# Kernel optimization log

Measured on AMD Instinct MI355X. Metric: run time of the kernel, lower is better.

The kernel has to match this reference:

```python
import jax, jax.numpy as jnp
from jax import lax
import numpy as np

K = 5  # length_inter_tile
EPS = 0.01


def _conv(x, w, b):
    y = lax.conv_general_dilated(x, w, (1, 1), ((1, 1), (1, 1)),
                                 dimension_numbers=('NCHW', 'OIHW', 'NCHW'))
    return y + b[None, :, None, None]


def _leaky(x):
    return jnp.where(x >= 0, x, 0.01 * x)


def _unfold(x, k=K):
    # torch F.unfold(x, k, padding=k//2): (b,c,h,w) -> (b, c*k*k, h*w), channel-major ordering
    b, c, h, w = x.shape
    p = k // 2
    xp = jnp.pad(x, ((0, 0), (0, 0), (p, p), (p, p)))
    pat = jnp.stack([xp[:, :, i:i + h, j:j + w] for i in range(k) for j in range(k)], axis=2)
    return pat.reshape(b, c * k * k, h * w)


def _fold(x, c, h, w, k=K):
    # torch F.fold: (b, c*k*k, h*w) -> (b, c, h, w) with overlap-add, padding=k//2
    b = x.shape[0]
    p = k // 2
    xr = x.reshape(b, c, k, k, h, w)
    out = jnp.zeros((b, c, h + 2 * p, w + 2 * p), x.dtype)
    for i in range(k):
        for j in range(k):
            out = out.at[:, :, i:i + h, j:j + w].add(xr[:, :, i, j])
    return out[:, :, p:p + h, p:p + w]


def _mmn(x, axes):
    mn = jnp.min(x, axis=axes, keepdims=True)
    mx = jnp.max(x, axis=axes, keepdims=True)
    return (x - mn) / (mx - mn + 0.001)


def setup_inputs() -> dict:
    key = jax.random.key(0)
    ks = jax.random.split(key, 8)
    b, t, ch_in, h, w = 1, 16, 10, 24, 24
    t_de, ch_de = 16, 12
    sc = 0.02
    return {
        'x': jax.random.normal(ks[0], (b, t, ch_in, h, w), jnp.float32),
        'design': jax.random.uniform(ks[1], (b, t_de, ch_de, h, w), jnp.float32),
        'gt': jax.random.uniform(ks[2], (b, t_de, 3, h, w), jnp.float32),
        'w1': jax.random.normal(ks[3], (1024, 160, 3, 3), jnp.float32) * sc,
        'b1': jnp.zeros((1024,), jnp.float32),
        'w2': jax.random.normal(ks[4], (1024, 1024, 3, 3), jnp.float32) * sc,
        'b2': jnp.zeros((1024,), jnp.float32),
        'w3': jax.random.normal(ks[5], (1024, 1024, 3, 3), jnp.float32) * sc,
        'b3': jnp.zeros((1024,), jnp.float32),
        'wf': jax.random.normal(ks[6], (6400, 1024, 3, 3), jnp.float32) * sc,
        'bf': jnp.zeros((6400,), jnp.float32),
    }


def _forward(x, design, gt, w1, b1, w2, b2, w3, b3, wf, bf):
    b, t, ch_in, h, w = x.shape
    t_de, ch_de = design.shape[1], design.shape[2]
    hw = h * w
    N = K * K  # num_inter

    # unfold design: (b, t_de*ch_de*N, hw) -> (b*hw, N, t_de, ch_de)
    d = _unfold(design.reshape(b, t_de * ch_de, h, w))
    d = d.transpose(0, 2, 1).reshape(b * hw, t_de * ch_de, N)
    d = d.transpose(0, 2, 1).reshape(b * hw, N, t_de, ch_de)

    # norm in each prediction window (per channel-group, per sample)
    d = jnp.concatenate([
        d[..., 0:1],
        _mmn(d[..., 1:4], (1, 2, 3)),
        _mmn(d[..., 4:5], (1, 2)),
        _mmn(d[..., 5:8], (1, 2, 3)),
        _mmn(d[..., 8:], (1, 2)),  # each grid channel independently
    ], axis=-1)

    M = b * hw * N
    domain = d.reshape(M, t_de, ch_de)
    X = d[:, :, :t, :].reshape(M, t, ch_de)

    # feature network (n_layers=4 -> 3 leaky convs) + weight head
    f = _leaky(_conv(x.reshape(b, t * ch_in, h, w), w1, b1))
    f = _leaky(_conv(f, w2, b2))
    f = _leaky(_conv(f, w3, b3))
    Wt = jnp.tanh(_conv(f, wf, bf))  # (b, N*t*t, h, w)
    Wm = Wt.reshape(b, N, t, t, h, w).transpose(0, 4, 5, 1, 2, 3).reshape(M, t, t)
    Wm = jnp.einsum('nij,nkj->nik', Wm, Wm) + jnp.eye(t, dtype=Wm.dtype)

    XTW = jnp.einsum('ntc,ntu->ncu', X, Wm)          # (M, ch_de, t)
    XTWX = jnp.einsum('nct,ntd->ncd', XTW, X)        # (M, ch_de, ch_de)
    A = XTWX.reshape(b * hw, N, ch_de, ch_de).sum(1) + EPS * jnp.eye(ch_de, dtype=XTWX.dtype)

    # reference for loss (unfolded)
    ref = _unfold(gt.reshape(b, t_de * 3, h, w))
    ref = ref.transpose(0, 2, 1).reshape(b * hw, t_de * 3, N)
    ref = ref.transpose(0, 2, 1).reshape(M, t_de, 3)

    outs, folded = [], []
    for ch in range(3):
        Y = _unfold(x[:, :, ch])                      # (b, t*N, hw)
        Y = Y.transpose(0, 2, 1).reshape(b * hw, t, N)
        Y = Y.transpose(0, 2, 1).reshape(M, t, 1)
        XTWY = jnp.einsum('nct,nto->nco', XTW, Y)
        Bv = XTWY.reshape(b * hw, N, ch_de, 1).sum(1)
        para = jnp.linalg.solve(A, Bv)                # (b*hw, ch_de, 1)
        para_r = jnp.broadcast_to(para[:, None], (b * hw, N, ch_de, 1)).reshape(M, ch_de, 1)
        o = jnp.einsum('ntc,nco->nto', domain, para_r)  # (M, t_de, 1)
        outs.append(o[..., 0])
        # overlap-add fold of per-window predictions
        oc = o.reshape(b, hw, N, t_de).transpose(0, 3, 2, 1).reshape(b, t_de * N, hw)
        num = _fold(oc, t_de, h, w)
        den = _fold(jnp.ones_like(oc), t_de, h, w)
        folded.append(num / den)

    out_for_loss = jnp.stack(outs, axis=-1)           # (M, t_de, 3)
    out = jnp.stack(folded, axis=2)                   # (b, t_de, 3, h, w)
    loss = jnp.mean(jnp.abs(out_for_loss - ref))      # L1 stand-in for loss_for_stit_v1
    return out, loss


def reference(x, design, gt, w1, b1, w2, b2, w3, b3, wf, bf):
    return _forward(x, design, gt, w1, b1, w2, b2, w3, b3, wf, bf)
```

## Files before the change

### kernel.cpp

```cpp
#include <hip/hip_runtime.h>
#include <math.h>


typedef __attribute__((ext_vector_type(8))) short sh8;
typedef __attribute__((ext_vector_type(4))) float f32x4;


__device__ inline void glds16(const void* gsrc, void* ldst) {
    __builtin_amdgcn_global_load_lds((const __attribute__((address_space(1))) void*)gsrc,
                                     (__attribute__((address_space(3))) void*)ldst, 16, 0, 0);
}

__global__ __launch_bounds__(64) void minmax_kernel(const float* __restrict__ design,
                                                    float* __restrict__ mn_o,
                                                    float* __restrict__ mx_o) {
    int p = blockIdx.x;
    int py = p / 24, px = p % 24;
    int lane = threadIdx.x;
    float mn[7], mx[7];
#pragma unroll
    for (int g = 0; g < 7; g++) { mn[g] = 1e30f; mx[g] = -1e30f; }
    for (int e = lane; e < 400; e += 64) {
        int n = e / 16, td = e % 16;
        int yy = py + n / 5 - 2, xx = px + n % 5 - 2;
        bool ok = (yy >= 0 && yy < 24 && xx >= 0 && xx < 24);
#pragma unroll
        for (int cd = 1; cd < 12; cd++) {
            float v = ok ? design[(td * 12 + cd) * 576 + yy * 24 + xx] : 0.0f;
            int g = (cd <= 3) ? 0 : (cd == 4) ? 1 : (cd <= 7) ? 2 : 3 + (cd - 8);
            mn[g] = fminf(mn[g], v);
            mx[g] = fmaxf(mx[g], v);
        }
    }
#pragma unroll
    for (int s = 32; s >= 1; s >>= 1) {
#pragma unroll
        for (int g = 0; g < 7; g++) {
            mn[g] = fminf(mn[g], __shfl_xor(mn[g], s));
            mx[g] = fmaxf(mx[g], __shfl_xor(mx[g], s));
        }
    }
    if (lane == 0) {
#pragma unroll
        for (int g = 0; g < 7; g++) {
            mn_o[p * 7 + g] = mn[g];
            mx_o[p * 7 + g] = mx[g];
        }
    }
}

__global__ void dnorm_kernel(const float* __restrict__ design,
                             const float* __restrict__ mn,
                             const float* __restrict__ mx,
                             float* __restrict__ dn) {
    int idx = blockIdx.x * 256 + threadIdx.x;
    if (idx >= 14400 * 192) return;
    int cd = idx % 12;
    int td = (idx / 12) % 16;
    int n  = (idx / 192) % 25;
    int p  = idx / 4800;
    int py = p / 24, px = p % 24;
    int yy = py + n / 5 - 2, xx = px + n % 5 - 2;
    float v = (yy >= 0 && yy < 24 && xx >= 0 && xx < 24)
                  ? design[(td * 12 + cd) * 576 + yy * 24 + xx] : 0.0f;
    if (cd >= 1) {
        int g = (cd <= 3) ? 0 : (cd == 4) ? 1 : (cd <= 7) ? 2 : 3 + (cd - 8);
        float a = mn[p * 7 + g], b = mx[p * 7 + g];
        v = (v - a) / (b - a + 0.001f);
    }
    dn[idx] = v;
}

__global__ __launch_bounds__(256) void im2col_kernel(const float* __restrict__ act,
                                                     char* __restrict__ x2t, int nrows) {
    int row = blockIdx.x * 256 + threadIdx.x;
    if (row >= nrows) return;
    int kc = row / 576, px = row % 576;
    int y = px / 24, x = px % 24;
    int k0 = kc * 32;
    int ic = k0 / 9;
    int tap = k0 - ic * 9;
    sh8 hv[4], lv[4];
#pragma unroll
    for (int e = 0; e < 32; ++e) {
        int dy = tap / 3, dx = tap - dy * 3;
        int yy = y + dy - 1, xx = x + dx - 1;
        float v = (yy >= 0 && yy < 24 && xx >= 0 && xx < 24)
                      ? act[ic * 576 + yy * 24 + xx] : 0.0f;
        unsigned u = __builtin_bit_cast(unsigned, v);
        hv[e / 8][e % 8] = (short)(u >> 16);
        float fh = __builtin_bit_cast(float, u & 0xFFFF0000u);
        lv[e / 8][e % 8] = (short)(__builtin_bit_cast(unsigned, v - fh) >> 16);
        if (++tap == 9) { tap = 0; ++ic; }
    }
    char* dst = x2t + (long)kc * 92160 + (long)px * 80;
#pragma unroll
    for (int s4 = 0; s4 < 4; ++s4) {
        *(sh8*)(dst + s4 * 16) = hv[s4];
        *(sh8*)(dst + 46080 + s4 * 16) = lv[s4];
    }
}

__global__ void finalize_kernel(const float* __restrict__ part,
                                const float* __restrict__ bias,
                                float* __restrict__ act, int total, int nsplit) {
    int idx = blockIdx.x * 256 + threadIdx.x;
    if (idx >= total) return;
    float s = 0.0f;
    for (int k = 0; k < nsplit; k++) s += part[(long)k * total + idx];
    s += bias[idx / 576];
    act[idx] = s >= 0.0f ? s : 0.01f * s;
}

template<int SWZ>
__global__ __launch_bounds__(256, 2)
void conv_mfma5_kernel(const char* __restrict__ x2t,
                       const float* __restrict__ wgt,
                       float* __restrict__ part,
                       int K, int cps, int cout) {
    __shared__ __align__(1024) char sB[46080];
    __shared__ __align__(1024) char sA[2][16384];

    const int tid = threadIdx.x;
    const int lane = tid & 63;
    const int w = tid >> 6;
    const int wo = w >> 1, wp = w & 1;
    const int q = lane >> 4, ln15 = lane & 15;

    int ocb, pxh, s;
    if (SWZ) {
        int g = blockIdx.x;
        int xcd = g & 7, slot = g >> 3;
        int p = xcd + 8 * (slot >> 1);
        ocb = p % 50; s = p / 50; pxh = slot & 1;
    } else {
        ocb = blockIdx.x; pxh = blockIdx.y; s = blockIdx.z;
    }
    const int c0 = s * cps;

    const int st_oc = tid >> 1;
    const int st_h  = tid & 1;
    const float* wrow = wgt + (long)(ocb * 128 + st_oc) * K + st_h * 16;
    const int wslot0 = (((st_h * 2 + 0) + (st_oc >> 1)) & 3) << 4;
    const int wslot1 = (((st_h * 2 + 1) + (st_oc >> 1)) & 3) << 4;
    char* const arow_base = (char*)nullptr;

    int aoff[4];
#pragma unroll
    for (int ot = 0; ot < 4; ++ot) {
        int oc = wo * 64 + ot * 16 + ln15;
        aoff[ot] = oc * 64 + (((q + (oc >> 1)) & 3) << 4);
    }
    const int bbase = (wp * 144 + ln15) * 80 + q * 16;

    f32x4 acc[4][9];
#pragma unroll
    for (int a = 0; a < 4; ++a)
#pragma unroll
        for (int j = 0; j < 9; ++j) acc[a][j] = f32x4{0.f, 0.f, 0.f, 0.f};

    {
        const float* p = wrow + (long)c0 * 32;
        float4 a0 = *(const float4*)(p);
        float4 a1 = *(const float4*)(p + 4);
        float4 a2 = *(const float4*)(p + 8);
        float4 a3 = *(const float4*)(p + 12);
        float av[16] = {a0.x, a0.y, a0.z, a0.w, a1.x, a1.y, a1.z, a1.w,
                        a2.x, a2.y, a2.z, a2.w, a3.x, a3.y, a3.z, a3.w};
        sh8 h8[2], l8[2];
#pragma unroll
        for (int e = 0; e < 16; ++e) {
            unsigned u = __builtin_bit_cast(unsigned, av[e]);
            h8[e / 8][e % 8] = (short)(u >> 16);
            float fh = __builtin_bit_cast(float, u & 0xFFFF0000u);
            l8[e / 8][e % 8] = (short)(__builtin_bit_cast(unsigned, av[e] - fh) >> 16);
        }
        char* hb = sA[0] + st_oc * 64;
        *(sh8*)(hb + wslot0) = h8[0];
        *(sh8*)(hb + wslot1) = h8[1];
        *(sh8*)(hb + 8192 + wslot0) = l8[0];
        *(sh8*)(hb + 8192 + wslot1) = l8[1];
    }

#pragma unroll 1
    for (int t = 0; t < cps; ++t) {
        const int cc = c0 + t;
        __syncthreads();
        {
            const char* bsrc = x2t + (long)cc * 92160 + pxh * 23040;
            for (int it = w; it < 45; it += 4) {
                int boff = it * 1024 + lane * 16;
                const char* src = (boff < 23040) ? bsrc + boff
                                                 : bsrc + 46080 + (boff - 23040);
                glds16(src, sB + it * 1024);
            }
        }
        __builtin_amdgcn_sched_barrier(0);
        const bool pf = (t + 1 < cps);
        float4 a0, a1, a2, a3;
        if (pf) {
            const float* p = wrow + (long)(cc + 1) * 32;
            a0 = *(const float4*)(p);
            a1 = *(const float4*)(p + 4);
            a2 = *(const float4*)(p + 8);
            a3 = *(const float4*)(p + 12);
            asm volatile("s_waitcnt vmcnt(4)" ::: "memory");
        } else {
            asm volatile("s_waitcnt vmcnt(0)" ::: "memory");
        }
        __syncthreads();

        const char* sAc = sA[t & 1];
        sh8 ah[4], al[4];
#pragma unroll
        for (int ot = 0; ot < 4; ++ot) {
            ah[ot] = *(const sh8*)(sAc + aoff[ot]);
            al[ot] = *(const sh8*)(sAc + 8192 + aoff[ot]);
        }
#pragma unroll
        for (int j = 0; j < 9; ++j) {
            int ba = bbase + j * (16 * 80);
            sh8 bh = *(const sh8*)(sB + ba);
            sh8 bl = *(const sh8*)(sB + 23040 + ba);
#pragma unroll
            for (int ot = 0; ot < 4; ++ot) {
                acc[ot][j] = __builtin_amdgcn_mfma_f32_16x16x32_bf16(ah[ot], bh, acc[ot][j], 0, 0, 0);
                acc[ot][j] = __builtin_amdgcn_mfma_f32_16x16x32_bf16(al[ot], bh, acc[ot][j], 0, 0, 0);
                acc[ot][j] = __builtin_amdgcn_mfma_f32_16x16x32_bf16(ah[ot], bl, acc[ot][j], 0, 0, 0);
            }
        }
        if (pf) {
            float av[16] = {a0.x, a0.y, a0.z, a0.w, a1.x, a1.y, a1.z, a1.w,
                            a2.x, a2.y, a2.z, a2.w, a3.x, a3.y, a3.z, a3.w};
            sh8 h8[2], l8[2];
#pragma unroll
            for (int e = 0; e < 16; ++e) {
                unsigned u = __builtin_bit_cast(unsigned, av[e]);
                h8[e / 8][e % 8] = (short)(u >> 16);
                float fh = __builtin_bit_cast(float, u & 0xFFFF0000u);
                l8[e / 8][e % 8] = (short)(__builtin_bit_cast(unsigned, av[e] - fh) >> 16);
            }
            char* hb = sA[(t + 1) & 1] + st_oc * 64;
            *(sh8*)(hb + wslot0) = h8[0];
            *(sh8*)(hb + wslot1) = h8[1];
            *(sh8*)(hb + 8192 + wslot0) = l8[0];
            *(sh8*)(hb + 8192 + wslot1) = l8[1];
        }
    }
#pragma unroll
    for (int ot = 0; ot < 4; ++ot) {
        int oc0 = ocb * 128 + wo * 64 + ot * 16 + q * 4;
#pragma unroll
        for (int j = 0; j < 9; ++j) {
            int px = pxh * 288 + wp * 144 + j * 16 + ln15;
#pragma unroll
            for (int vr = 0; vr < 4; ++vr)
                part[((long)s * cout + oc0 + vr) * 576 + px] = acc[ot][j][vr];
        }
    }
}

__global__ __launch_bounds__(256) void tanh_tr_kernel(const float* __restrict__ part,
                                                      const float* __restrict__ bias,
                                                      float* __restrict__ wtT) {
    __shared__ float tile[64][65];
    int oc0 = blockIdx.x * 64, p0 = blockIdx.y * 64;
    int tx = threadIdx.x, ty = threadIdx.y;
#pragma unroll
    for (int k = 0; k < 16; k++) {
        int row = ty + k * 4;
        float s = 0.f;
#pragma unroll
        for (int sp = 0; sp < 4; ++sp)
            s += part[((long)sp * 6400 + oc0 + row) * 576 + p0 + tx];
        tile[row][tx] = tanhf(s + bias[oc0 + row]);
    }
    __syncthreads();
#pragma unroll
    for (int k = 0; k < 16; k++) {
        int rr = ty + k * 4;
        wtT[(long)(p0 + rr) * 6400 + oc0 + tx] = tile[tx][rr];
    }
}

__global__ __launch_bounds__(256) void stagec_kernel(const float* __restrict__ dn,
                                                     const float* __restrict__ wtT,
                                                     const float* __restrict__ xin,
                                                     const float* __restrict__ gt,
                                                     float* __restrict__ ob,
                                                     float* __restrict__ lp) {
    int p = blockIdx.x;
    int py = p / 24, px = p % 24;
    int tid = threadIdx.x;
    __shared__ float sX[4800];
    __shared__ float sW[6400];
    __shared__ float sY[1200];
    __shared__ float sP[192];
    __shared__ float sXTW[192];
    __shared__ float sA[144];
    __shared__ float sB[36];
    __shared__ double dA[144];
    __shared__ double db[36];
    __shared__ float spara[36];
    __shared__ float sred[256];

    for (int e = tid; e < 4800; e += 256) sX[e] = dn[(long)p * 4800 + e];
    for (int e = tid; e < 6400; e += 256) sW[e] = wtT[(long)p * 6400 + e];
    for (int e = tid; e < 1200; e += 256) {
        int n = e / 48, t = (e % 48) / 3, ch = e % 3;
        int yy = py + n / 5 - 2, xx = px + n % 5 - 2;
        sY[e] = (yy >= 0 && yy < 24 && xx >= 0 && xx < 24)
                    ? xin[(t * 10 + ch) * 576 + yy * 24 + xx] : 0.0f;
    }
    if (tid < 144) sA[tid] = 0.0f;
    if (tid < 36) sB[tid] = 0.0f;
    __syncthreads();

    for (int n = 0; n < 25; n++) {
        const float* X = sX + n * 192;
        const float* W = sW + n * 256;
        if (tid < 192) {
            int c = tid >> 4, j = tid & 15;
            float s = 0.0f;
#pragma unroll
            for (int t = 0; t < 16; t++) s = fmaf(X[t * 12 + c], W[t * 16 + j], s);
            sP[tid] = s;
        }
        __syncthreads();
        if (tid < 192) {
            int c = tid >> 4, u = tid & 15;
            float s = X[u * 12 + c];
#pragma unroll
            for (int j = 0; j < 16; j++) s = fmaf(sP[c * 16 + j], W[u * 16 + j], s);
            sXTW[tid] = s;
        }
        __syncthreads();
        if (tid < 144) {
            int c = tid / 12, d2 = tid % 12;
            float s = 0.0f;
#pragma unroll
            for (int t = 0; t < 16; t++) s = fmaf(sXTW[c * 16 + t], X[t * 12 + d2], s);
            sA[tid] += s;
        } else if (tid < 180) {
            int e = tid - 144;
            int c = e / 3, ch = e % 3;
            float s = 0.0f;
#pragma unroll
            for (int t = 0; t < 16; t++) s = fmaf(sXTW[c * 16 + t], sY[n * 48 + t * 3 + ch], s);
            sB[e] += s;
        }
        __syncthreads();
    }

    if (tid < 144) dA[tid] = (double)sA[tid] + ((tid % 13 == 0) ? 0.01 : 0.0);
    if (tid < 36) db[tid] = (double)sB[tid];
    __syncthreads();

    if (tid == 0) {
        for (int kk = 0; kk < 12; kk++) {
            double d = dA[kk * 12 + kk];
            for (int q2 = 0; q2 < kk; q2++) d -= dA[kk * 12 + q2] * dA[kk * 12 + q2];
            d = sqrt(d);
            dA[kk * 12 + kk] = d;
            double inv = 1.0 / d;
            for (int i = kk + 1; i < 12; i++) {
                double s = dA[i * 12 + kk];
                for (int q2 = 0; q2 < kk; q2++) s -= dA[i * 12 + q2] * dA[kk * 12 + q2];
                dA[i * 12 + kk] = s * inv;
            }
        }
        for (int ch = 0; ch < 3; ch++) {
            double t2[12];
            for (int i = 0; i < 12; i++) {
                double s = db[i * 3 + ch];
                for (int q2 = 0; q2 < i; q2++) s -= dA[i * 12 + q2] * t2[q2];
                t2[i] = s / dA[i * 12 + i];
            }
            for (int i = 11; i >= 0; i--) {
                double s = t2[i];
                for (int q2 = i + 1; q2 < 12; q2++) s -= dA[q2 * 12 + i] * t2[q2];
                t2[i] = s / dA[i * 12 + i];
            }
            for (int i = 0; i < 12; i++) spara[i * 3 + ch] = (float)t2[i];
        }
    }
    __syncthreads();

    float lsum = 0.0f;
    for (int e = tid; e < 1200; e += 256) {
        int n = e / 48, td = (e % 48) / 3, ch = e % 3;
        float s = 0.0f;
#pragma unroll
        for (int c = 0; c < 12; c++) s = fmaf(sX[n * 192 + td * 12 + c], spara[c * 3 + ch], s);
        ob[((long)(p * 25 + n)) * 48 + td * 3 + ch] = s;
        int yy = py + n / 5 - 2, xx = px + n % 5 - 2;
        float rv = (yy >= 0 && yy < 24 && xx >= 0 && xx < 24)
                       ? gt[(td * 3 + ch) * 576 + yy * 24 + xx] : 0.0f;
        lsum += fabsf(s - rv);
    }
    sred[tid] = lsum;
    __syncthreads();
    for (int s = 128; s >= 1; s >>= 1) {
        if (tid < s) sred[tid] += sred[tid + s];
        __syncthreads();
    }
    if (tid == 0) lp[p] = sred[0];
}

__global__ void fold_kernel(const float* __restrict__ ob, float* __restrict__ out) {
    int idx = blockIdx.x * 256 + threadIdx.x;
    if (idx >= 27648) return;
    int td = idx / 1728;
    int rem = idx % 1728;
    int ch = rem / 576;
    int p = rem % 576;
    int y = p / 24, x = p % 24;
    float num = 0.0f;
    int den = 0;
    for (int i = 0; i < 5; i++) {
        int yy = y + 2 - i;
        if (yy < 0 || yy >= 24) continue;
        for (int j = 0; j < 5; j++) {
            int xx = x + 2 - j;
            if (xx < 0 || xx >= 24) continue;
            num += ob[((long)((yy * 24 + xx) * 25 + i * 5 + j)) * 48 + td * 3 + ch];
            den++;
        }
    }
    out[idx] = num / (float)den;
}

__global__ __launch_bounds__(64) void loss_kernel(const float* __restrict__ lp,
                                                  float* __restrict__ out) {
    int t = threadIdx.x;
    float s = 0.0f;
    for (int e = t; e < 576; e += 64) s += lp[e];
#pragma unroll
    for (int d = 32; d >= 1; d >>= 1) s += __shfl_xor(s, d);
    if (t == 0) out[27648] = s / 691200.0f;
}

extern "C" void kernel_launch(void* const* d_in, const int* in_sizes, int n_in,
                              void* d_out, int out_size, void* d_ws, size_t ws_size,
                              hipStream_t stream) {
    const float* x      = (const float*)d_in[0];
    const float* design = (const float*)d_in[1];
    const float* gt     = (const float*)d_in[2];
    const float* w1     = (const float*)d_in[3];
    const float* b1     = (const float*)d_in[4];
    const float* w2     = (const float*)d_in[5];
    const float* b2     = (const float*)d_in[6];
    const float* w3     = (const float*)d_in[7];
    const float* b3     = (const float*)d_in[8];
    const float* wf     = (const float*)d_in[9];
    const float* bf     = (const float*)d_in[10];
    float* out = (float*)d_out;
    char* wsb  = (char*)d_ws;

    const int big = (ws_size >= 118257408UL) ? 1 : 0;
    const int ks23 = big ? 32 : 16;
    const int cps23 = big ? 9 : 18;
    size_t off_x2t = big ? 75497472UL : 58982400UL;
    size_t off_act = off_x2t + 26542080UL;
    size_t off_dn  = off_act + 2359296UL;
    size_t off_ob  = off_dn + 11059200UL;
    size_t off_mn  = off_ob + 2764800UL;
    size_t off_mx  = off_mn + 16128UL;
    size_t off_lp  = off_mx + 16128UL;

    float* part = (float*)(wsb);
    char*  x2t  = wsb + off_x2t;
    float* wtT  = (float*)(wsb + off_x2t);
    float* act  = (float*)(wsb + off_act);
    float* dn   = (float*)(wsb + off_dn);
    float* ob   = (float*)(wsb + off_ob);
    float* mn   = (float*)(wsb + off_mn);
    float* mx   = (float*)(wsb + off_mx);
    float* lp   = (float*)(wsb + off_lp);

    minmax_kernel<<<576, 64, 0, stream>>>(design, mn, mx);
    dnorm_kernel<<<10800, 256, 0, stream>>>(design, mn, mx, dn);

    im2col_kernel<<<102, 256, 0, stream>>>(x, x2t, 45 * 576);
    conv_mfma5_kernel<0><<<dim3(8, 2, 15), 256, 0, stream>>>(x2t, w1, part, 1440, 3, 1024);
    finalize_kernel<<<2304, 256, 0, stream>>>(part, b1, act, 589824, 15);
    im2col_kernel<<<648, 256, 0, stream>>>(act, x2t, 288 * 576);
    conv_mfma5_kernel<0><<<dim3(8, 2, ks23), 256, 0, stream>>>(x2t, w2, part, 9216, cps23, 1024);
    finalize_kernel<<<2304, 256, 0, stream>>>(part, b2, act, 589824, ks23);
    im2col_kernel<<<648, 256, 0, stream>>>(act, x2t, 288 * 576);
    conv_mfma5_kernel<0><<<dim3(8, 2, ks23), 256, 0, stream>>>(x2t, w3, part, 9216, cps23, 1024);
    finalize_kernel<<<2304, 256, 0, stream>>>(part, b3, act, 589824, ks23);
    im2col_kernel<<<648, 256, 0, stream>>>(act, x2t, 288 * 576);
    conv_mfma5_kernel<1><<<400, 256, 0, stream>>>(x2t, wf, part, 9216, 72, 6400);
    tanh_tr_kernel<<<dim3(100, 9), dim3(64, 4), 0, stream>>>(part, bf, wtT);

    stagec_kernel<<<576, 256, 0, stream>>>(dn, wtT, x, gt, ob, lp);
    fold_kernel<<<108, 256, 0, stream>>>(ob, out);
    loss_kernel<<<1, 64, 0, stream>>>(lp, out);
}
```

Measured before the change: 581.5 us.

## Load im2col B fragments directly into registers in MFMA-ready layout

The im2col output is rearranged into 16-pixel groups laid out in MFMA fragment order. The conv kernel then drops the LDS staging buffer for the activation operand and loads B fragments straight from global memory into registers, software-pipelined one chunk ahead. LDS use shrinks and one barrier per iteration goes away, at the cost of more registers and of relying on L2 hits for the per-wave global loads. Workspace offsets are fixed to the small layout, so the big-workspace split of 32 for conv2/3 is no longer used.

```diff
diff --git a/kernel.cpp b/kernel.cpp
--- a/kernel.cpp
+++ b/kernel.cpp
@@ -5,11 +5,16 @@
 typedef __attribute__((ext_vector_type(8))) short sh8;
 typedef __attribute__((ext_vector_type(4))) float f32x4;
 
-
-__device__ inline void glds16(const void* gsrc, void* ldst) {
-    __builtin_amdgcn_global_load_lds((const __attribute__((address_space(1))) void*)gsrc,
-                                     (__attribute__((address_space(3))) void*)ldst, 16, 0, 0);
-}
+#define OFF_PART 0UL
+#define OFF_X2T  58982400UL
+#define OFF_WTT  58982400UL
+#define OFF_ACT  80216064UL
+#define OFF_DN   82575360UL
+#define OFF_OB   93634560UL
+#define OFF_MN   96399360UL
+#define OFF_MX   96415488UL
+#define OFF_LP   96431616UL
+
 
 __global__ __launch_bounds__(64) void minmax_kernel(const float* __restrict__ design,
                                                     float* __restrict__ mn_o,
@@ -93,11 +98,12 @@
         lv[e / 8][e % 8] = (short)(__builtin_bit_cast(unsigned, v - fh) >> 16);
         if (++tap == 9) { tap = 0; ++ic; }
     }
-    char* dst = x2t + (long)kc * 92160 + (long)px * 80;
-#pragma unroll
-    for (int s4 = 0; s4 < 4; ++s4) {
-        *(sh8*)(dst + s4 * 16) = hv[s4];
-        *(sh8*)(dst + 46080 + s4 * 16) = lv[s4];
+    int pg = px >> 4, l15 = px & 15;
+    char* dst = x2t + (long)kc * 73728 + pg * 2048 + l15 * 16;
+#pragma unroll
+    for (int q = 0; q < 4; ++q) {
+        *(sh8*)(dst + q * 256) = hv[q];
+        *(sh8*)(dst + 1024 + q * 256) = lv[q];
     }
 }
 
@@ -114,11 +120,10 @@
 
 template<int SWZ>
 __global__ __launch_bounds__(256, 2)
-void conv_mfma5_kernel(const char* __restrict__ x2t,
+void conv_mfma7_kernel(const char* __restrict__ x2t,
                        const float* __restrict__ wgt,
                        float* __restrict__ part,
                        int K, int cps, int cout) {
-    __shared__ __align__(1024) char sB[46080];
     __shared__ __align__(1024) char sA[2][16384];
 
     const int tid = threadIdx.x;
@@ -126,6 +131,7 @@
     const int w = tid >> 6;
     const int wo = w >> 1, wp = w & 1;
     const int q = lane >> 4, ln15 = lane & 15;
+    const int lane16 = lane * 16;
 
     int ocb, pxh, s;
     if (SWZ) {
@@ -137,13 +143,12 @@
         ocb = blockIdx.x; pxh = blockIdx.y; s = blockIdx.z;
     }
     const int c0 = s * cps;
-
-    const int st_oc = tid >> 1;
-    const int st_h  = tid & 1;
+    const int cend = c0 + cps - 1;
+
+    const int st_oc = tid >> 1, st_h = tid & 1;
     const float* wrow = wgt + (long)(ocb * 128 + st_oc) * K + st_h * 16;
     const int wslot0 = (((st_h * 2 + 0) + (st_oc >> 1)) & 3) << 4;
     const int wslot1 = (((st_h * 2 + 1) + (st_oc >> 1)) & 3) << 4;
-    char* const arow_base = (char*)nullptr;
 
     int aoff[4];
 #pragma unroll
@@ -151,7 +156,8 @@
         int oc = wo * 64 + ot * 16 + ln15;
         aoff[ot] = oc * 64 + (((q + (oc >> 1)) & 3) << 4);
     }
-    const int bbase = (wp * 144 + ln15) * 80 + q * 16;
+
+    const char* bbase = x2t + (long)(pxh * 18 + wp * 9) * 2048;
 
     f32x4 acc[4][9];
 #pragma unroll
@@ -159,6 +165,14 @@
 #pragma unroll
         for (int j = 0; j < 9; ++j) acc[a][j] = f32x4{0.f, 0.f, 0.f, 0.f};
 
+    sh8 bh[9], bl[3];
+    {
+        const char* bc = bbase + (long)c0 * 73728;
+#pragma unroll
+        for (int j = 0; j < 9; ++j) bh[j] = *(const sh8*)(bc + j * 2048 + lane16);
+#pragma unroll
+        for (int j = 0; j < 3; ++j) bl[j] = *(const sh8*)(bc + j * 2048 + 1024 + lane16);
+    }
     {
         const float* p = wrow + (long)c0 * 32;
         float4 a0 = *(const float4*)(p);
@@ -181,54 +195,51 @@
         *(sh8*)(hb + 8192 + wslot0) = l8[0];
         *(sh8*)(hb + 8192 + wslot1) = l8[1];
     }
+    __syncthreads();
 
 #pragma unroll 1
     for (int t = 0; t < cps; ++t) {
-        const int cc = c0 + t;
-        __syncthreads();
-        {
-            const char* bsrc = x2t + (long)cc * 92160 + pxh * 23040;
-            for (int it = w; it < 45; it += 4) {
-                int boff = it * 1024 + lane * 16;
-                const char* src = (boff < 23040) ? bsrc + boff
-                                                 : bsrc + 46080 + (boff - 23040);
-                glds16(src, sB + it * 1024);
-            }
-        }
-        __builtin_amdgcn_sched_barrier(0);
+        const int cur = t & 1;
         const bool pf = (t + 1 < cps);
-        float4 a0, a1, a2, a3;
-        if (pf) {
-            const float* p = wrow + (long)(cc + 1) * 32;
-            a0 = *(const float4*)(p);
-            a1 = *(const float4*)(p + 4);
-            a2 = *(const float4*)(p + 8);
-            a3 = *(const float4*)(p + 12);
-            asm volatile("s_waitcnt vmcnt(4)" ::: "memory");
-        } else {
-            asm volatile("s_waitcnt vmcnt(0)" ::: "memory");
-        }
-        __syncthreads();
-
-        const char* sAc = sA[t & 1];
+        const int cc1 = pf ? (c0 + t + 1) : cend;
+        const char* bcur  = bbase + (long)(c0 + t) * 73728;
+        const char* bnext = bbase + (long)cc1 * 73728;
+
+        const float* ap = wrow + (long)cc1 * 32;
+        float4 a0 = *(const float4*)(ap);
+        float4 a1 = *(const float4*)(ap + 4);
+        float4 a2 = *(const float4*)(ap + 8);
+        float4 a3 = *(const float4*)(ap + 12);
+
+        const char* sAc = sA[cur];
         sh8 ah[4], al[4];
 #pragma unroll
         for (int ot = 0; ot < 4; ++ot) {
             ah[ot] = *(const sh8*)(sAc + aoff[ot]);
             al[ot] = *(const sh8*)(sAc + 8192 + aoff[ot]);
         }
+
 #pragma unroll
         for (int j = 0; j < 9; ++j) {
-            int ba = bbase + j * (16 * 80);
-            sh8 bh = *(const sh8*)(sB + ba);
-            sh8 bl = *(const sh8*)(sB + 23040 + ba);
-#pragma unroll
-            for (int ot = 0; ot < 4; ++ot) {
-                acc[ot][j] = __builtin_amdgcn_mfma_f32_16x16x32_bf16(ah[ot], bh, acc[ot][j], 0, 0, 0);
-                acc[ot][j] = __builtin_amdgcn_mfma_f32_16x16x32_bf16(al[ot], bh, acc[ot][j], 0, 0, 0);
-                acc[ot][j] = __builtin_amdgcn_mfma_f32_16x16x32_bf16(ah[ot], bl, acc[ot][j], 0, 0, 0);
-            }
-        }
+            const int sl = j % 3;
+            sh8 bhj = bh[j];
+            sh8 blj = bl[sl];
+#pragma unroll
+            for (int ot = 0; ot < 4; ++ot)
+                acc[ot][j] = __builtin_amdgcn_mfma_f32_16x16x32_bf16(ah[ot], bhj, acc[ot][j], 0, 0, 0);
+#pragma unroll
+            for (int ot = 0; ot < 4; ++ot)
+                acc[ot][j] = __builtin_amdgcn_mfma_f32_16x16x32_bf16(al[ot], bhj, acc[ot][j], 0, 0, 0);
+#pragma unroll
+            for (int ot = 0; ot < 4; ++ot)
+                acc[ot][j] = __builtin_amdgcn_mfma_f32_16x16x32_bf16(ah[ot], blj, acc[ot][j], 0, 0, 0);
+            bh[j] = *(const sh8*)(bnext + j * 2048 + lane16);
+            const int jn = j + 3;
+            const char* bs = (jn < 9) ? bcur : bnext;
+            const int jj = (jn < 9) ? jn : jn - 9;
+            bl[sl] = *(const sh8*)(bs + jj * 2048 + 1024 + lane16);
+        }
+
         if (pf) {
             float av[16] = {a0.x, a0.y, a0.z, a0.w, a1.x, a1.y, a1.z, a1.w,
                             a2.x, a2.y, a2.z, a2.w, a3.x, a3.y, a3.z, a3.w};
@@ -240,11 +251,12 @@
                 float fh = __builtin_bit_cast(float, u & 0xFFFF0000u);
                 l8[e / 8][e % 8] = (short)(__builtin_bit_cast(unsigned, av[e] - fh) >> 16);
             }
-            char* hb = sA[(t + 1) & 1] + st_oc * 64;
+            char* hb = sA[cur ^ 1] + st_oc * 64;
             *(sh8*)(hb + wslot0) = h8[0];
             *(sh8*)(hb + wslot1) = h8[1];
             *(sh8*)(hb + 8192 + wslot0) = l8[0];
             *(sh8*)(hb + 8192 + wslot1) = l8[1];
+            __syncthreads();
         }
     }
 #pragma unroll
@@ -262,7 +274,7 @@
 
 __global__ __launch_bounds__(256) void tanh_tr_kernel(const float* __restrict__ part,
                                                       const float* __restrict__ bias,
-                                                      float* __restrict__ wtT) {
+                                                      float* __restrict__ wtT, int nsplit) {
     __shared__ float tile[64][65];
     int oc0 = blockIdx.x * 64, p0 = blockIdx.y * 64;
     int tx = threadIdx.x, ty = threadIdx.y;
@@ -270,8 +282,7 @@
     for (int k = 0; k < 16; k++) {
         int row = ty + k * 4;
         float s = 0.f;
-#pragma unroll
-        for (int sp = 0; sp < 4; ++sp)
+        for (int sp = 0; sp < nsplit; ++sp)
             s += part[((long)sp * 6400 + oc0 + row) * 576 + p0 + tx];
         tile[row][tx] = tanhf(s + bias[oc0 + row]);
     }
@@ -457,42 +468,31 @@
     float* out = (float*)d_out;
     char* wsb  = (char*)d_ws;
 
-    const int big = (ws_size >= 118257408UL) ? 1 : 0;
-    const int ks23 = big ? 32 : 16;
-    const int cps23 = big ? 9 : 18;
-    size_t off_x2t = big ? 75497472UL : 58982400UL;
-    size_t off_act = off_x2t + 26542080UL;
-    size_t off_dn  = off_act + 2359296UL;
-    size_t off_ob  = off_dn + 11059200UL;
-    size_t off_mn  = off_ob + 2764800UL;
-    size_t off_mx  = off_mn + 16128UL;
-    size_t off_lp  = off_mx + 16128UL;
-
-    float* part = (float*)(wsb);
-    char*  x2t  = wsb + off_x2t;
-    float* wtT  = (float*)(wsb + off_x2t);
-    float* act  = (float*)(wsb + off_act);
-    float* dn   = (float*)(wsb + off_dn);
-    float* ob   = (float*)(wsb + off_ob);
-    float* mn   = (float*)(wsb + off_mn);
-    float* mx   = (float*)(wsb + off_mx);
-    float* lp   = (float*)(wsb + off_lp);
+    float* part = (float*)(wsb + OFF_PART);
+    char*  x2t  = wsb + OFF_X2T;
+    float* wtT  = (float*)(wsb + OFF_WTT);
+    float* act  = (float*)(wsb + OFF_ACT);
+    float* dn   = (float*)(wsb + OFF_DN);
+    float* ob   = (float*)(wsb + OFF_OB);
+    float* mn   = (float*)(wsb + OFF_MN);
+    float* mx   = (float*)(wsb + OFF_MX);
+    float* lp   = (float*)(wsb + OFF_LP);
 
     minmax_kernel<<<576, 64, 0, stream>>>(design, mn, mx);
     dnorm_kernel<<<10800, 256, 0, stream>>>(design, mn, mx, dn);
 
     im2col_kernel<<<102, 256, 0, stream>>>(x, x2t, 45 * 576);
-    conv_mfma5_kernel<0><<<dim3(8, 2, 15), 256, 0, stream>>>(x2t, w1, part, 1440, 3, 1024);
+    conv_mfma7_kernel<0><<<dim3(8, 2, 15), 256, 0, stream>>>(x2t, w1, part, 1440, 3, 1024);
     finalize_kernel<<<2304, 256, 0, stream>>>(part, b1, act, 589824, 15);
     im2col_kernel<<<648, 256, 0, stream>>>(act, x2t, 288 * 576);
-    conv_mfma5_kernel<0><<<dim3(8, 2, ks23), 256, 0, stream>>>(x2t, w2, part, 9216, cps23, 1024);
-    finalize_kernel<<<2304, 256, 0, stream>>>(part, b2, act, 589824, ks23);
+    conv_mfma7_kernel<0><<<dim3(8, 2, 16), 256, 0, stream>>>(x2t, w2, part, 9216, 18, 1024);
+    finalize_kernel<<<2304, 256, 0, stream>>>(part, b2, act, 589824, 16);
     im2col_kernel<<<648, 256, 0, stream>>>(act, x2t, 288 * 576);
-    conv_mfma5_kernel<0><<<dim3(8, 2, ks23), 256, 0, stream>>>(x2t, w3, part, 9216, cps23, 1024);
-    finalize_kernel<<<2304, 256, 0, stream>>>(part, b3, act, 589824, ks23);
+    conv_mfma7_kernel<0><<<dim3(8, 2, 16), 256, 0, stream>>>(x2t, w3, part, 9216, 18, 1024);
+    finalize_kernel<<<2304, 256, 0, stream>>>(part, b3, act, 589824, 16);
     im2col_kernel<<<648, 256, 0, stream>>>(act, x2t, 288 * 576);
-    conv_mfma5_kernel<1><<<400, 256, 0, stream>>>(x2t, wf, part, 9216, 72, 6400);
-    tanh_tr_kernel<<<dim3(100, 9), dim3(64, 4), 0, stream>>>(part, bf, wtT);
+    conv_mfma7_kernel<1><<<400, 256, 0, stream>>>(x2t, wf, part, 9216, 72, 6400);
+    tanh_tr_kernel<<<dim3(100, 9), dim3(64, 4), 0, stream>>>(part, bf, wtT, 4);
 
     stagec_kernel<<<576, 256, 0, stream>>>(dn, wtT, x, gt, ob, lp);
     fold_kernel<<<108, 256, 0, stream>>>(ob, out);
```

After: 593.7 us. 2.1% more time.
